# Optimization experiments

Measured on AMD Instinct MI355X. Metric: run time of the kernel, lower is better.

## Reference

```python
import jax, jax.numpy as jnp
from jax import lax
import numpy as np

B, N, D_MODEL = 4, 2048, 768
D_INNER = 1536      # int(2.0 * d_model)
DT_RANK = 48        # ceil(768 / 16)
EPS = 1e-5


def setup_inputs() -> dict:
    key = jax.random.key(0)
    ks = jax.random.split(key, 9)
    x = jax.random.normal(ks[0], (B, N, D_MODEL), jnp.float32)
    # BFS order: a permutation of node ids
    sorted_index = jax.random.permutation(ks[1], N).astype(jnp.int32)
    # parent BFS position of node at BFS position i, must be < i; root (i=0) has -1
    pos = jnp.arange(N)
    r = jax.random.randint(ks[2], (N,), 0, N)
    sorted_parent = jnp.where(pos == 0, -1, r % jnp.maximum(pos, 1)).astype(jnp.int32)
    s = 0.02
    in_proj_w = jax.random.normal(ks[3], (D_MODEL, 2 * D_INNER), jnp.float32) * s
    x_proj_w = jax.random.normal(ks[4], (D_INNER, DT_RANK + 2), jnp.float32) * s
    dt_proj_w = jax.random.normal(ks[5], (DT_RANK, D_INNER), jnp.float32) * (DT_RANK ** -0.5)
    # dt bias init: softplus^{-1}(dt) with dt ~ LogUniform(1e-3, 1e-1)
    dt = jnp.exp(jax.random.uniform(ks[6], (D_INNER,)) * (np.log(0.1) - np.log(0.001)) + np.log(0.001))
    dt_proj_b = (dt + jnp.log(-jnp.expm1(-dt))).astype(jnp.float32)
    A_log = jnp.zeros((D_INNER,), jnp.float32)   # log(A=1) per original init (d_state=1)
    D_param = jnp.ones((D_INNER,), jnp.float32)
    ln_gamma = jnp.ones((D_INNER,), jnp.float32)
    ln_beta = jnp.zeros((D_INNER,), jnp.float32)
    out_proj_w = jax.random.normal(ks[7], (D_INNER, D_MODEL), jnp.float32) * s
    return dict(x=x, sorted_index=sorted_index, sorted_parent=sorted_parent,
                in_proj_w=in_proj_w, x_proj_w=x_proj_w, dt_proj_w=dt_proj_w,
                dt_proj_b=dt_proj_b, A_log=A_log, D_param=D_param,
                ln_gamma=ln_gamma, ln_beta=ln_beta, out_proj_w=out_proj_w)


def _tree_ssm_recurrence(dBx, dA, sorted_index, sorted_parent):
    """h[bfs i] = dA[node(i)] * h[parent_bfs(i)] + dBx[node(i)]. Inputs (B,N,Di) node-major."""
    b, n, di = dBx.shape
    dA_bfs = jnp.take(dA, sorted_index, axis=1)    # (B,N,Di) in BFS order
    dBx_bfs = jnp.take(dBx, sorted_index, axis=1)

    def step(h_buf, inp):
        t, par, dA_t, dBx_t = inp                   # dA_t/dBx_t: (B,Di)
        h_par = h_buf[:, jnp.maximum(par, 0)]       # (B,Di) gather at parent BFS pos
        h_par = jnp.where(par < 0, jnp.zeros_like(h_par), h_par)
        h_t = dA_t * h_par + dBx_t
        return h_buf.at[:, t].set(h_t), h_t

    xs = (jnp.arange(n), sorted_parent,
          dA_bfs.transpose(1, 0, 2), dBx_bfs.transpose(1, 0, 2))
    _, h_bfs = lax.scan(step, jnp.zeros((b, n, di), dBx.dtype), xs)
    # scatter BFS-order states back to node-id order
    h = jnp.zeros((b, n, di), dBx.dtype).at[:, sorted_index].set(h_bfs.transpose(1, 0, 2))
    return h


def reference(x, sorted_index, sorted_parent, in_proj_w, x_proj_w, dt_proj_w,
              dt_proj_b, A_log, D_param, ln_gamma, ln_beta, out_proj_w):
    xz = x @ in_proj_w                              # (B,N,2*Di)
    x_inner, z = jnp.split(xz, 2, axis=-1)
    z = jax.nn.silu(z)
    x_dbl = x_inner @ x_proj_w                      # (B,N,dt_rank+2)
    dt_lr, B_ssm, C_ssm = (x_dbl[..., :DT_RANK], x_dbl[..., DT_RANK:DT_RANK + 1],
                           x_dbl[..., DT_RANK + 1:DT_RANK + 2])
    dt = jax.nn.softplus(dt_lr @ dt_proj_w + dt_proj_b)  # (B,N,Di)
    As = -jnp.exp(A_log)                            # (Di,) negative
    dA = jnp.exp(dt * As)                           # (B,N,Di) in (0,1)
    dBx = dt * B_ssm * x_inner                      # (B,N,Di)
    h = _tree_ssm_recurrence(dBx, dA, sorted_index, sorted_parent)
    y = h * C_ssm + D_param * x_inner               # (B,N,Di)
    mu = jnp.mean(y, axis=-1, keepdims=True)
    var = jnp.mean(jnp.square(y - mu), axis=-1, keepdims=True)
    y = (y - mu) * lax.rsqrt(var + EPS) * ln_gamma + ln_beta
    y = y * z
    return y @ out_proj_w                           # (B,N,D)
```

## Files before the change

### kernel.cpp

```cpp
#include <hip/hip_runtime.h>
#include <math.h>


#define ROWS 8192
#define DIN 1536
#define DMOD 768
#define NSEQ 2048
#define DTR 48
#define NSPLIT 4

typedef __bf16 bfrag __attribute__((ext_vector_type(8)));
typedef float f4 __attribute__((ext_vector_type(4)));

__device__ __forceinline__ unsigned short f2bf(float f) {
  unsigned int u = __float_as_uint(f);
  unsigned int r = (u + 0x7fffu + ((u >> 16) & 1u)) >> 16;
  return (unsigned short)r;
}
__device__ __forceinline__ float bf2f(unsigned short h) {
  return __uint_as_float(((unsigned int)h) << 16);
}

__device__ __forceinline__ void gld_lds16(const void* g, void* l) {
  __builtin_amdgcn_global_load_lds((const __attribute__((address_space(1))) void*)g,
                                   (__attribute__((address_space(3))) void*)l, 16, 0, 0);
}

__device__ __forceinline__ void barx() {
  asm volatile("" ::: "memory");
  __builtin_amdgcn_s_barrier();
  asm volatile("" ::: "memory");
}

__global__ __launch_bounds__(512, 1) void gemm256_silu(
    const unsigned short* __restrict__ A, const unsigned short* __restrict__ Bt,
    unsigned short* __restrict__ XI, unsigned short* __restrict__ Z, int K) {
  __shared__ unsigned short lds[2][(256 + 192) * 64];
  const int tid = threadIdx.x;
  const int w = tid >> 6, l = tid & 63;
  const int quad = l >> 4, l16 = l & 15;
  const int wr = w >> 2, wc = w & 3;
  const int h = blockIdx.x + 16 * blockIdx.y;
  const int swz = (h & 7) * 64 + (h >> 3);
  const int row0 = (swz >> 4) * 256, col0 = (swz & 15) * 192;
  const int nt = K >> 6;

  const int srow = tid >> 3;
  const int schunk = ((tid & 7) ^ (srow & 7)) * 8;
  const unsigned short* aS = A + (size_t)(row0 + srow) * K + schunk;
  const unsigned short* bS = Bt + (size_t)(col0 + srow) * K + schunk;

#define STG_A(bufi, q, kt)                                     \
  gld_lds16(aS + (size_t)((q) * 64) * K + (size_t)(kt) * 64,   \
            (char*)&lds[bufi][(q) * 4096] + w * 1024)
#define STG_B(bufi, q, kt)                                     \
  gld_lds16(bS + (size_t)((q) * 64) * K + (size_t)(kt) * 64,   \
            (char*)&lds[bufi][16384 + (q) * 4096] + w * 1024)

  const int arow = (wr * 128 + l16) * 64;
  const int brow = (wc * 48 + l16) * 64;
  int cs[2];
  cs[0] = (quad ^ (l16 & 7)) * 8;
  cs[1] = ((4 + quad) ^ (l16 & 7)) * 8;

#define RDA(m, ks) (*(const bfrag*)(const void*)(LA + arow + (m) * 1024 + cs[ks]))
#define RDB(n, ks) (*(const bfrag*)(const void*)(LB + brow + (n) * 1024 + cs[ks]))

  f4 acc[8][3];
#pragma unroll
  for (int m = 0; m < 8; m++)
#pragma unroll
    for (int n = 0; n < 3; n++) acc[m][n] = (f4){0.f, 0.f, 0.f, 0.f};

  const int kt1 = (nt > 1) ? 1 : 0;
#pragma unroll
  for (int q = 0; q < 4; q++) STG_A(0, q, 0);
#pragma unroll
  for (int q = 0; q < 3; q++) STG_B(0, q, 0);
#pragma unroll
  for (int q = 0; q < 4; q++) STG_A(1, q, kt1);
#pragma unroll
  for (int q = 0; q < 3; q++) STG_B(1, q, kt1);
  asm volatile("s_waitcnt vmcnt(7)" ::: "memory");
  barx();

  for (int t = 0; t < nt; ++t) {
    const int b = t & 1;
    const unsigned short* LA = &lds[b][0];
    const unsigned short* LB = &lds[b][16384];
    const int kA = (t + 2 < nt) ? (t + 2) : (nt - 1);
    bfrag af[4][2], bfr[3][2];

#pragma unroll
    for (int m = 0; m < 4; m++) {
      af[m][0] = RDA(m, 0);
      af[m][1] = RDA(m, 1);
    }
#pragma unroll
    for (int n = 0; n < 3; n++) {
      bfr[n][0] = RDB(n, 0);
      bfr[n][1] = RDB(n, 1);
    }
    barx();
    __builtin_amdgcn_s_setprio(1);
#pragma unroll
    for (int m = 0; m < 4; m++)
#pragma unroll
      for (int n = 0; n < 3; n++) {
        acc[m][n] = __builtin_amdgcn_mfma_f32_16x16x32_bf16(af[m][0], bfr[n][0], acc[m][n], 0, 0, 0);
        acc[m][n] = __builtin_amdgcn_mfma_f32_16x16x32_bf16(af[m][1], bfr[n][1], acc[m][n], 0, 0, 0);
      }
    __builtin_amdgcn_s_setprio(0);
    barx();

#pragma unroll
    for (int m = 0; m < 4; m++) {
      af[m][0] = RDA(m + 4, 0);
      af[m][1] = RDA(m + 4, 1);
    }
    STG_A(b, 0, kA);
    STG_A(b, 2, kA);
    STG_B(b, 0, kA);
    STG_B(b, 1, kA);
    STG_B(b, 2, kA);
    barx();
    STG_A(b, 1, kA);
    STG_A(b, 3, kA);
    __builtin_amdgcn_s_setprio(1);
#pragma unroll
    for (int m = 0; m < 4; m++)
#pragma unroll
      for (int n = 0; n < 3; n++) {
        acc[m + 4][n] = __builtin_amdgcn_mfma_f32_16x16x32_bf16(af[m][0], bfr[n][0], acc[m + 4][n], 0, 0, 0);
        acc[m + 4][n] = __builtin_amdgcn_mfma_f32_16x16x32_bf16(af[m][1], bfr[n][1], acc[m + 4][n], 0, 0, 0);
      }
    __builtin_amdgcn_s_setprio(0);
    asm volatile("s_waitcnt vmcnt(7)" ::: "memory");
    barx();
  }
  asm volatile("s_waitcnt vmcnt(0)" ::: "memory");

#undef STG_A
#undef STG_B
#undef RDA
#undef RDB

  const bool is_z = (col0 >= DIN);
  unsigned short* dst = is_z ? Z : XI;
  const int cb = col0 + wc * 48 + l16 - (is_z ? DIN : 0);
#pragma unroll
  for (int m = 0; m < 8; m++) {
    const int rb = row0 + wr * 128 + m * 16 + quad * 4;
#pragma unroll
    for (int n = 0; n < 3; n++)
#pragma unroll
      for (int r = 0; r < 4; r++) {
        float v = acc[m][n][r];
        if (is_z) v = v / (1.f + __expf(-v));
        dst[(size_t)(rb + r) * DIN + cb + n * 16] = f2bf(v);
      }
  }
}

template <int MODE>
__global__ __launch_bounds__(256) void mfma_gemm(
    const unsigned short* __restrict__ A, const unsigned short* __restrict__ Bt,
    void* __restrict__ C0v, void* __restrict__ C1v, int K, int ldc) {
  __shared__ unsigned short As[128 * 32];
  __shared__ unsigned short Bs[128 * 32];
  const int tid = threadIdx.x;
  const int w = tid >> 6, l = tid & 63;
  const int quad = l >> 4, l16 = l & 15;
  const int wrow = (w >> 1) * 64, wcol = (w & 1) * 64;
  const int h = blockIdx.x + gridDim.x * blockIdx.y;
  const int nb = gridDim.x * gridDim.y;
  int swz = h;
  if ((nb & 7) == 0) swz = (h & 7) * (nb >> 3) + (h >> 3);
  const int row0 = (swz / gridDim.x) * 128, col0 = (swz % gridDim.x) * 128;

  f4 acc[4][4];
#pragma unroll
  for (int i = 0; i < 4; i++)
#pragma unroll
    for (int j = 0; j < 4; j++) acc[i][j] = (f4){0.f, 0.f, 0.f, 0.f};

  const int arow = row0 + w * 16 + (l >> 2);
  const int brow = col0 + w * 16 + (l >> 2);
  const int kcol = (((l & 3) ^ ((l >> 2) & 3)) * 8);
  const int qs = (quad ^ (l16 & 3)) * 8;

  for (int k0 = 0; k0 < K; k0 += 32) {
#pragma unroll
    for (int r = 0; r < 2; r++) {
      gld_lds16(A + (size_t)(arow + r * 64) * K + k0 + kcol,
                (char*)As + r * 4096 + w * 1024);
      gld_lds16(Bt + (size_t)(brow + r * 64) * K + k0 + kcol,
                (char*)Bs + r * 4096 + w * 1024);
    }
    __syncthreads();
    bfrag af[4], bf[4];
#pragma unroll
    for (int i = 0; i < 4; i++)
      af[i] = *(const bfrag*)(const void*)(As + (wrow + i * 16 + l16) * 32 + qs);
#pragma unroll
    for (int j = 0; j < 4; j++)
      bf[j] = *(const bfrag*)(const void*)(Bs + (wcol + j * 16 + l16) * 32 + qs);
#pragma unroll
    for (int i = 0; i < 4; i++)
#pragma unroll
      for (int j = 0; j < 4; j++)
        acc[i][j] = __builtin_amdgcn_mfma_f32_16x16x32_bf16(af[i], bf[j], acc[i][j], 0, 0, 0);
    __syncthreads();
  }

  if (MODE == 0) {
    float* C0 = (float*)C0v;
    const int ccol = col0 + wcol + l16;
#pragma unroll
    for (int i = 0; i < 4; i++) {
      const int rb = row0 + wrow + i * 16 + quad * 4;
#pragma unroll
      for (int j = 0; j < 4; j++)
#pragma unroll
        for (int r = 0; r < 4; r++)
          C0[(size_t)(rb + r) * ldc + ccol + j * 16] = acc[i][j][r];
    }
  } else {
    const bool is_z = (col0 >= DIN);
    unsigned short* dst = is_z ? (unsigned short*)C1v : (unsigned short*)C0v;
    const int cbase = col0 + wcol + l16 - (is_z ? DIN : 0);
#pragma unroll
    for (int i = 0; i < 4; i++) {
      const int rb = row0 + wrow + i * 16 + quad * 4;
#pragma unroll
      for (int j = 0; j < 4; j++)
#pragma unroll
        for (int r = 0; r < 4; r++) {
          float v = acc[i][j][r];
          if (is_z) v = v / (1.f + __expf(-v));
          dst[(size_t)(rb + r) * DIN + cbase + j * 16] = f2bf(v);
        }
    }
  }
}

__global__ __launch_bounds__(1024) void prep1_kernel(
    const int* __restrict__ sidx, const int* __restrict__ spar,
    int* __restrict__ SLOT_PACK, int* __restrict__ SLOTINV,
    int* __restrict__ LSTART, int* __restrict__ NLEV,
    const float* __restrict__ x, unsigned short* __restrict__ Xbf,
    const float* __restrict__ xpw, unsigned short* __restrict__ XPW,
    const float* __restrict__ dtw, unsigned short* __restrict__ DTWb,
    const float* __restrict__ A_log, float* __restrict__ negA) {
  const int bi = blockIdx.x;
  const int tid = threadIdx.x;
  if (bi == 0) {
    __shared__ int par[2048], idx[2048], ancA[2048], ancB[2048], rnkA[2048], rnkB[2048];
    __shared__ int dmax;
    for (int i = tid; i < 2048; i += 1024) {
      const int p = spar[i];
      par[i] = p;
      idx[i] = sidx[i];
      ancA[i] = (p < 0) ? -1 : p;
      rnkA[i] = (p < 0) ? 0 : 1;
    }
    if (tid == 0) dmax = 0;
    __syncthreads();
    for (int r = 0; r < 11; r++) {
      int* ca = (r & 1) ? ancB : ancA;
      int* cr = (r & 1) ? rnkB : rnkA;
      int* na = (r & 1) ? ancA : ancB;
      int* nr = (r & 1) ? rnkA : rnkB;
      for (int i = tid; i < 2048; i += 1024) {
        const int a = ca[i], rv = cr[i];
        if (a >= 0) {
          nr[i] = rv + cr[a];
          na[i] = ca[a];
        } else {
          nr[i] = rv;
          na[i] = a;
        }
      }
      __syncthreads();
    }
    for (int i = tid; i < 2048; i += 1024) ancA[i] = 0;
    __syncthreads();
    for (int i = tid; i < 2048; i += 1024) {
      atomicAdd(&ancA[rnkB[i]], 1);
      atomicMax(&dmax, rnkB[i]);
    }
    __syncthreads();
    for (int s = 0; s < 11; s++) {
      const int off = 1 << s;
      int* cur = (s & 1) ? ancB : ancA;
      int* nxt = (s & 1) ? ancA : ancB;
      for (int i = tid; i < 2048; i += 1024) {
        int v = cur[i];
        if (i >= off) v += cur[i - off];
        nxt[i] = v;
      }
      __syncthreads();
    }
    for (int i = tid; i < 2049; i += 1024) {
      const int v = (i == 0) ? 0 : ancB[i - 1];
      LSTART[i] = v;
      if (i < 2048) rnkA[i] = v;
    }
    if (tid == 0) NLEV[0] = dmax + 1;
    __syncthreads();
    for (int i = tid; i < 2048; i += 1024) {
      const int d = rnkB[i];
      const int slot = atomicAdd(&rnkA[d], 1);
      const int node = idx[i];
      const int p = par[i];
      const int pn = (p < 0) ? -1 : idx[p];
      SLOT_PACK[slot] = node | ((pn + 1) << 12);
      SLOTINV[node] = slot;
    }
  } else if (bi < 1 + 1536) {
    const int i = ((bi - 1) * 1024 + tid) * 4;
    const float4 v = *(const float4*)(x + i);
    union { unsigned short h[4]; uint2 u; } pk;
    pk.h[0] = f2bf(v.x);
    pk.h[1] = f2bf(v.y);
    pk.h[2] = f2bf(v.z);
    pk.h[3] = f2bf(v.w);
    *(uint2*)(Xbf + i) = pk.u;
  } else if (bi < 1 + 1536 + 96) {
    const int i = (bi - 1537) * 1024 + tid;
    const int c = i / 1536, k = i % 1536;
    XPW[i] = (c < 50) ? f2bf(xpw[(size_t)k * 50 + c]) : (unsigned short)0;
  } else if (bi < 1 + 1536 + 96 + 96) {
    const int i = (bi - 1633) * 1024 + tid;
    const int d = i >> 6, k = i & 63;
    DTWb[i] = (k < 48) ? f2bf(dtw[(size_t)k * DIN + d]) : (unsigned short)0;
  } else {
    const int i = (bi - 1729) * 1024 + tid;
    if (i < DIN) negA[i] = -__expf(A_log[i]);
  }
}

__global__ __launch_bounds__(256) void prep2_kernel(
    const float* __restrict__ W1, unsigned short* __restrict__ W1t,
    const float* __restrict__ W2, unsigned short* __restrict__ W2t) {
  __shared__ float t[32][33];
  int idx = blockIdx.x;
  const float* W;
  unsigned short* Wt;
  int K, N, n0, k0;
  if (idx < 2304) {
    W = W1; Wt = W1t; K = DMOD; N = 2 * DIN;
    n0 = (idx % 96) * 32; k0 = (idx / 96) * 32;
  } else {
    idx -= 2304;
    W = W2; Wt = W2t; K = DIN; N = DMOD;
    n0 = (idx % 24) * 32; k0 = (idx / 24) * 32;
  }
  const int tx = threadIdx.x & 31, ty = threadIdx.x >> 5;
  for (int i = ty; i < 32; i += 8) t[i][tx] = W[(size_t)(k0 + i) * N + n0 + tx];
  __syncthreads();
  for (int i = ty; i < 32; i += 8)
    Wt[(size_t)(n0 + i) * K + k0 + tx] = f2bf(t[tx][i]);
}

__global__ __launch_bounds__(256) void xdbl_mfma(
    const unsigned short* __restrict__ XI, const unsigned short* __restrict__ XPW,
    float* __restrict__ XP) {
  __shared__ unsigned short As[128 * 32];
  __shared__ unsigned short Bs[64 * 32];
  const int tid = threadIdx.x;
  const int w = tid >> 6, l = tid & 63;
  const int quad = l >> 4, l16 = l & 15;
  const int h = blockIdx.x + 4 * blockIdx.y;
  const int swz = (h & 7) * 32 + (h >> 3);
  const int split = swz & 3;
  const int row0 = (swz >> 2) * 128;
  const int kbase = split * (DIN / NSPLIT);

  f4 acc[2][4];
#pragma unroll
  for (int i = 0; i < 2; i++)
#pragma unroll
    for (int j = 0; j < 4; j++) acc[i][j] = (f4){0.f, 0.f, 0.f, 0.f};

  const int srow = w * 16 + (l >> 2);
  const int kcol = (((l & 3) ^ ((l >> 2) & 3)) * 8);
  const int qs = (quad ^ (l16 & 3)) * 8;

  for (int c = 0; c < 12; c++) {
    const int k0 = kbase + c * 32;
#pragma unroll
    for (int r = 0; r < 2; r++) {
      gld_lds16(XI + (size_t)(row0 + srow + r * 64) * DIN + k0 + kcol,
                (char*)As + r * 4096 + w * 1024);
    }
    gld_lds16(XPW + (size_t)srow * DIN + k0 + kcol, (char*)Bs + w * 1024);
    __syncthreads();
    bfrag af[2], bf[4];
#pragma unroll
    for (int i = 0; i < 2; i++)
      af[i] = *(const bfrag*)(const void*)(As + (w * 32 + i * 16 + l16) * 32 + qs);
#pragma unroll
    for (int j = 0; j < 4; j++)
      bf[j] = *(const bfrag*)(const void*)(Bs + (j * 16 + l16) * 32 + qs);
#pragma unroll
    for (int i = 0; i < 2; i++)
#pragma unroll
      for (int j = 0; j < 4; j++)
        acc[i][j] = __builtin_amdgcn_mfma_f32_16x16x32_bf16(af[i], bf[j], acc[i][j], 0, 0, 0);
    __syncthreads();
  }

  float* dst = XP + (size_t)split * ROWS * 64 + (size_t)row0 * 64;
#pragma unroll
  for (int i = 0; i < 2; i++) {
    const int rb = w * 32 + i * 16 + quad * 4;
#pragma unroll
    for (int j = 0; j < 4; j++) {
      const int col = j * 16 + l16;
#pragma unroll
      for (int r = 0; r < 4; r++) dst[(size_t)(rb + r) * 64 + col] = acc[i][j][r];
    }
  }
}

__global__ __launch_bounds__(256) void xp_reduce(
    const float* __restrict__ XP, unsigned short* __restrict__ DTLRb,
    float* __restrict__ BCv, float* __restrict__ CCv) {
  const int i = blockIdx.x * 256 + threadIdx.x;
  const int row = i >> 4, c4 = (i & 15) * 4;
  const float* p = XP + (size_t)row * 64 + c4;
  float4 s = make_float4(0.f, 0.f, 0.f, 0.f);
#pragma unroll
  for (int sp = 0; sp < NSPLIT; sp++) {
    const float4 v = *(const float4*)(p + (size_t)sp * ROWS * 64);
    s.x += v.x;
    s.y += v.y;
    s.z += v.z;
    s.w += v.w;
  }
  if (c4 == 48) {
    BCv[row] = s.x;
    CCv[row] = s.y;
  }
  union { unsigned short h[4]; uint2 u; } pk;
  pk.h[0] = f2bf(s.x);
  pk.h[1] = f2bf(s.y);
  pk.h[2] = f2bf(s.z);
  pk.h[3] = f2bf(s.w);
  *(uint2*)(DTLRb + (size_t)row * 64 + c4) = pk.u;
}

__global__ __launch_bounds__(256) void dt_gemm(
    const unsigned short* __restrict__ DTLRb, const unsigned short* __restrict__ DTWb,
    const float* __restrict__ bias, const float* __restrict__ negA,
    const float* __restrict__ BCv, const unsigned short* __restrict__ XI,
    const int* __restrict__ SLOTINV,
    unsigned short* __restrict__ DAp, unsigned short* __restrict__ DBXp) {
  __shared__ unsigned short As[2][64 * 32];
  __shared__ unsigned short Bs[2][128 * 32];
  __shared__ int sinv[64];
  __shared__ float bcs[64];
  const int tid = threadIdx.x;
  const int w = tid >> 6, l = tid & 63;
  const int quad = l >> 4, l16 = l & 15;
  const int wrow = (w >> 1) * 32, wcol = (w & 1) * 64;
  const int h = blockIdx.x + 12 * blockIdx.y;
  const int swz = (h & 7) * 192 + (h >> 3);
  const int row0 = (swz / 12) * 64, col0 = (swz % 12) * 128;
  const int p0 = row0 & (NSEQ - 1);
  const int bbase = row0 & ~(NSEQ - 1);
  const int srow = w * 16 + (l >> 2);
  const int koff = (((l & 3) ^ ((l >> 2) & 3)) * 8);
  const int qs = (quad ^ (l16 & 3)) * 8;

#pragma unroll
  for (int c = 0; c < 2; c++) {
    gld_lds16(DTLRb + (size_t)(row0 + srow) * 64 + c * 32 + koff,
              (char*)As[c] + w * 1024);
#pragma unroll
    for (int r = 0; r < 2; r++)
      gld_lds16(DTWb + (size_t)(col0 + srow + r * 64) * 64 + c * 32 + koff,
                (char*)Bs[c] + r * 4096 + w * 1024);
  }
  if (tid < 64) {
    sinv[tid] = SLOTINV[p0 + tid];
    bcs[tid] = BCv[row0 + tid];
  }
  __syncthreads();

  f4 acc[2][4];
#pragma unroll
  for (int i = 0; i < 2; i++)
#pragma unroll
    for (int j = 0; j < 4; j++) acc[i][j] = (f4){0.f, 0.f, 0.f, 0.f};

#pragma unroll
  for (int c = 0; c < 2; c++) {
    bfrag af[2], bf[4];
#pragma unroll
    for (int i = 0; i < 2; i++)
      af[i] = *(const bfrag*)(const void*)(As[c] + (wrow + i * 16 + l16) * 32 + qs);
#pragma unroll
    for (int j = 0; j < 4; j++)
      bf[j] = *(const bfrag*)(const void*)(Bs[c] + (wcol + j * 16 + l16) * 32 + qs);
#pragma unroll
    for (int i = 0; i < 2; i++)
#pragma unroll
      for (int j = 0; j < 4; j++)
        acc[i][j] = __builtin_amdgcn_mfma_f32_16x16x32_bf16(af[i], bf[j], acc[i][j], 0, 0, 0);
  }

  float bj[4], aj[4];
#pragma unroll
  for (int j = 0; j < 4; j++) {
    const int d = col0 + wcol + j * 16 + l16;
    bj[j] = bias[d];
    aj[j] = negA[d];
  }
#pragma unroll
  for (int i = 0; i < 2; i++) {
#pragma unroll
    for (int r = 0; r < 4; r++) {
      const int row_l = wrow + i * 16 + quad * 4 + r;
      const int row = row0 + row_l;
      const float bc = bcs[row_l];
      const size_t rp = (size_t)(bbase + sinv[row_l]) * DIN;
#pragma unroll
      for (int j = 0; j < 4; j++) {
        const int d = col0 + wcol + j * 16 + l16;
        const float s = acc[i][j][r] + bj[j];
        const float sp = fmaxf(s, 0.f) + __logf(1.f + __expf(-fabsf(s)));
        const float xi = bf2f(XI[(size_t)row * DIN + d]);
        DAp[rp + d] = f2bf(__expf(sp * aj[j]));
        DBXp[rp + d] = f2bf(sp * bc * xi);
      }
    }
  }
}

__global__ __launch_bounds__(256) void recur_kernel(
    const unsigned short* __restrict__ DAp, const unsigned short* __restrict__ DBXp,
    unsigned short* __restrict__ Hb,
    const int* __restrict__ SLOT_PACK, const int* __restrict__ LSTART,
    const int* __restrict__ NLEV) {
  __shared__ unsigned short hl[NSEQ * 16];
  __shared__ int spack[NSEQ];
  __shared__ int lst[258];
  const int tid = threadIdx.x;
  const int c8a = blockIdx.x * 2;
  const int b = c8a / 192;
  const int d8a = c8a % 192;
  const int nlev = NLEV[0];
  for (int i = tid; i < NSEQ; i += 256) spack[i] = SLOT_PACK[i];
  const int nl = (nlev + 1 < 258) ? nlev + 1 : 258;
  for (int i = tid; i < nl; i += 256) lst[i] = LSTART[i];
  __syncthreads();

  for (int L = 0; L < nlev; L++) {
    const int s0 = (L < 257) ? lst[L] : LSTART[L];
    const int s1 = (L + 1 < 258) ? lst[L + 1] : LSTART[L + 1];
    const int items = (s1 - s0) * 2;
    for (int it = tid; it < items; it += 256) {
      const int s = s0 + (it >> 1);
      const int ch = it & 1;
      const size_t goff = (size_t)(b * NSEQ + s) * DIN + (d8a + ch) * 8;
      union { uint4 u; unsigned short h[8]; } da, dbx, hpu, hvu;
      da.u = *(const uint4*)(DAp + goff);
      dbx.u = *(const uint4*)(DBXp + goff);
      const int pk = spack[s];
      const int node = pk & 4095;
      const int pn = (pk >> 12) - 1;
      float hp[8];
      if (pn >= 0) {
        hpu.u = *(const uint4*)(hl + pn * 16 + ch * 8);
#pragma unroll
        for (int e = 0; e < 8; e++) hp[e] = bf2f(hpu.h[e]);
      } else {
#pragma unroll
        for (int e = 0; e < 8; e++) hp[e] = 0.f;
      }
#pragma unroll
      for (int e = 0; e < 8; e++) {
        const float hv = fmaf(bf2f(da.h[e]), hp[e], bf2f(dbx.h[e]));
        hvu.h[e] = f2bf(hv);
      }
      *(uint4*)(hl + node * 16 + ch * 8) = hvu.u;
    }
    __syncthreads();
  }

  for (int i = tid; i < NSEQ * 2; i += 256) {
    const int node = i >> 1, ch = i & 1;
    *(uint4*)(Hb + (size_t)(b * NSEQ + node) * DIN + (d8a + ch) * 8) =
        *(const uint4*)(hl + node * 16 + ch * 8);
  }
}

__global__ __launch_bounds__(256) void ln_kernel(
    const unsigned short* __restrict__ Hb, const float* __restrict__ CCv,
    const unsigned short* __restrict__ XI, const float* __restrict__ Dp,
    const float* __restrict__ gamma, const float* __restrict__ beta,
    const unsigned short* __restrict__ Z, unsigned short* __restrict__ YLN) {
  const int row = blockIdx.x;
  const int tid = threadIdx.x;
  const float C = CCv[row];
  const unsigned short* hrow = Hb + (size_t)row * DIN;
  const unsigned short* xrow = XI + (size_t)row * DIN;
  float y[6];
  float s = 0.f, s2 = 0.f;
#pragma unroll
  for (int i = 0; i < 6; i++) {
    const int d = tid + i * 256;
    const float v = fmaf(bf2f(hrow[d]), C, Dp[d] * bf2f(xrow[d]));
    y[i] = v;
    s += v;
    s2 = fmaf(v, v, s2);
  }
#pragma unroll
  for (int off = 32; off >= 1; off >>= 1) {
    s += __shfl_down(s, off);
    s2 += __shfl_down(s2, off);
  }
  __shared__ float rs[4], rs2[4];
  const int w = tid >> 6;
  if ((tid & 63) == 0) {
    rs[w] = s;
    rs2[w] = s2;
  }
  __syncthreads();
  const float ts = rs[0] + rs[1] + rs[2] + rs[3];
  const float ts2 = rs2[0] + rs2[1] + rs2[2] + rs2[3];
  const float mu = ts * (1.f / 1536.f);
  const float var = ts2 * (1.f / 1536.f) - mu * mu;
  const float inv = rsqrtf(var + 1e-5f);
  unsigned short* yrow = YLN + (size_t)row * DIN;
  const unsigned short* zrow = Z + (size_t)row * DIN;
#pragma unroll
  for (int i = 0; i < 6; i++) {
    const int d = tid + i * 256;
    const float o = (y[i] - mu) * inv * gamma[d] + beta[d];
    yrow[d] = f2bf(o * bf2f(zrow[d]));
  }
}

extern "C" void kernel_launch(void* const* d_in, const int* in_sizes, int n_in,
                              void* d_out, int out_size, void* d_ws, size_t ws_size,
                              hipStream_t stream) {
  const float* x = (const float*)d_in[0];
  const int* sidx = (const int*)d_in[1];
  const int* spar = (const int*)d_in[2];
  const float* in_proj = (const float*)d_in[3];
  const float* x_proj = (const float*)d_in[4];
  const float* dt_proj = (const float*)d_in[5];
  const float* dt_b = (const float*)d_in[6];
  const float* A_log = (const float*)d_in[7];
  const float* Dp = (const float*)d_in[8];
  const float* gamma = (const float*)d_in[9];
  const float* beta = (const float*)d_in[10];
  const float* out_proj = (const float*)d_in[11];
  float* out = (float*)d_out;

  char* p = (char*)d_ws;
  const size_t RC = (size_t)ROWS * DIN;
  unsigned short* XI = (unsigned short*)p;   p += RC * 2;
  unsigned short* Z = (unsigned short*)p;    p += RC * 2;
  unsigned short* DAp = (unsigned short*)p;  p += RC * 2;
  unsigned short* DBXp = (unsigned short*)p; p += RC * 2;
  unsigned short* Hb = (unsigned short*)p;   p += RC * 2;
  float* XP = (float*)p;                     p += (size_t)NSPLIT * ROWS * 64 * 4;
  unsigned short* DTLRb = (unsigned short*)p; p += (size_t)ROWS * 64 * 2;
  float* BCv = (float*)p;                    p += ROWS * 4;
  float* CCv = (float*)p;                    p += ROWS * 4;
  float* negA = (float*)p;                   p += DIN * 4;
  unsigned short* Xbf = (unsigned short*)p;  p += (size_t)ROWS * DMOD * 2;
  unsigned short* W1t = (unsigned short*)p;  p += (size_t)2 * DIN * DMOD * 2;
  unsigned short* W2t = (unsigned short*)p;  p += (size_t)DMOD * DIN * 2;
  unsigned short* XPW = (unsigned short*)p;  p += (size_t)64 * DIN * 2;
  unsigned short* DTWb = (unsigned short*)p; p += (size_t)DIN * 64 * 2;
  int* ipart = (int*)p;
  int* SLOT_PACK = ipart;
  int* SLOTINV = ipart + 2048;
  int* LSTART = ipart + 4096;
  int* NLEV = ipart + 4096 + 2049;
  unsigned short* YLN = DAp;

  prep1_kernel<<<1731, 1024, 0, stream>>>(sidx, spar, SLOT_PACK, SLOTINV,
                                          LSTART, NLEV, x, Xbf, x_proj, XPW,
                                          dt_proj, DTWb, A_log, negA);
  prep2_kernel<<<3456, 256, 0, stream>>>(in_proj, W1t, out_proj, W2t);
  gemm256_silu<<<dim3(16, 32), 512, 0, stream>>>(Xbf, W1t, XI, Z, DMOD);
  xdbl_mfma<<<dim3(NSPLIT, 64), 256, 0, stream>>>(XI, XPW, XP);
  xp_reduce<<<ROWS * 16 / 256, 256, 0, stream>>>(XP, DTLRb, BCv, CCv);
  dt_gemm<<<dim3(12, 128), 256, 0, stream>>>(DTLRb, DTWb, dt_b, negA, BCv, XI,
                                             SLOTINV, DAp, DBXp);
  recur_kernel<<<384, 256, 0, stream>>>(DAp, DBXp, Hb, SLOT_PACK, LSTART, NLEV);
  ln_kernel<<<ROWS, 256, 0, stream>>>(Hb, CCv, XI, Dp, gamma, beta, Z, YLN);
  mfma_gemm<0><<<dim3(6, 64), 256, 0, stream>>>(YLN, W2t, out, nullptr, DIN, DMOD);
}
```

Before: 305.3 us.

## Replace output GEMM with double-buffered 128x192 tile kernel using 512 threads

The final out-projection GEMM moves from a simple 128x128-tile, 256-thread kernel with a BK=32 synchronous load-compute loop to a new kernel. The new kernel uses 512 threads, 128x192 tiles, BK=64 and two LDS buffers, prefetching the next K tiles with global_load_lds while MFMAs run under raised wave priority. The goal is to hide global-load latency and cut per-iteration barriers for the 8192x768x1536 GEMM. The grid shrinks to 256 blocks, which on a large GPU may leave compute units underused, and the larger LDS footprint may limit occupancy.

```diff
diff --git a/kernel.cpp b/kernel.cpp
--- a/kernel.cpp
+++ b/kernel.cpp
@@ -162,85 +162,110 @@
   }
 }
 
-template <int MODE>
-__global__ __launch_bounds__(256) void mfma_gemm(
+__global__ __launch_bounds__(512, 2) void gemm_out(
     const unsigned short* __restrict__ A, const unsigned short* __restrict__ Bt,
-    void* __restrict__ C0v, void* __restrict__ C1v, int K, int ldc) {
-  __shared__ unsigned short As[128 * 32];
-  __shared__ unsigned short Bs[128 * 32];
+    float* __restrict__ C0, int K, int ldc) {
+  __shared__ unsigned short lds[2][(128 + 192) * 64];
   const int tid = threadIdx.x;
   const int w = tid >> 6, l = tid & 63;
   const int quad = l >> 4, l16 = l & 15;
-  const int wrow = (w >> 1) * 64, wcol = (w & 1) * 64;
-  const int h = blockIdx.x + gridDim.x * blockIdx.y;
-  const int nb = gridDim.x * gridDim.y;
-  int swz = h;
-  if ((nb & 7) == 0) swz = (h & 7) * (nb >> 3) + (h >> 3);
-  const int row0 = (swz / gridDim.x) * 128, col0 = (swz % gridDim.x) * 128;
-
-  f4 acc[4][4];
-#pragma unroll
-  for (int i = 0; i < 4; i++)
-#pragma unroll
-    for (int j = 0; j < 4; j++) acc[i][j] = (f4){0.f, 0.f, 0.f, 0.f};
-
-  const int arow = row0 + w * 16 + (l >> 2);
-  const int brow = col0 + w * 16 + (l >> 2);
-  const int kcol = (((l & 3) ^ ((l >> 2) & 3)) * 8);
-  const int qs = (quad ^ (l16 & 3)) * 8;
-
-  for (int k0 = 0; k0 < K; k0 += 32) {
-#pragma unroll
-    for (int r = 0; r < 2; r++) {
-      gld_lds16(A + (size_t)(arow + r * 64) * K + k0 + kcol,
-                (char*)As + r * 4096 + w * 1024);
-      gld_lds16(Bt + (size_t)(brow + r * 64) * K + k0 + kcol,
-                (char*)Bs + r * 4096 + w * 1024);
-    }
-    __syncthreads();
-    bfrag af[4], bf[4];
-#pragma unroll
-    for (int i = 0; i < 4; i++)
-      af[i] = *(const bfrag*)(const void*)(As + (wrow + i * 16 + l16) * 32 + qs);
-#pragma unroll
-    for (int j = 0; j < 4; j++)
-      bf[j] = *(const bfrag*)(const void*)(Bs + (wcol + j * 16 + l16) * 32 + qs);
-#pragma unroll
-    for (int i = 0; i < 4; i++)
-#pragma unroll
-      for (int j = 0; j < 4; j++)
-        acc[i][j] = __builtin_amdgcn_mfma_f32_16x16x32_bf16(af[i], bf[j], acc[i][j], 0, 0, 0);
-    __syncthreads();
-  }
-
-  if (MODE == 0) {
-    float* C0 = (float*)C0v;
-    const int ccol = col0 + wcol + l16;
-#pragma unroll
-    for (int i = 0; i < 4; i++) {
-      const int rb = row0 + wrow + i * 16 + quad * 4;
-#pragma unroll
-      for (int j = 0; j < 4; j++)
-#pragma unroll
-        for (int r = 0; r < 4; r++)
-          C0[(size_t)(rb + r) * ldc + ccol + j * 16] = acc[i][j][r];
-    }
-  } else {
-    const bool is_z = (col0 >= DIN);
-    unsigned short* dst = is_z ? (unsigned short*)C1v : (unsigned short*)C0v;
-    const int cbase = col0 + wcol + l16 - (is_z ? DIN : 0);
-#pragma unroll
-    for (int i = 0; i < 4; i++) {
-      const int rb = row0 + wrow + i * 16 + quad * 4;
-#pragma unroll
-      for (int j = 0; j < 4; j++)
-#pragma unroll
-        for (int r = 0; r < 4; r++) {
-          float v = acc[i][j][r];
-          if (is_z) v = v / (1.f + __expf(-v));
-          dst[(size_t)(rb + r) * DIN + cbase + j * 16] = f2bf(v);
-        }
-    }
+  const int wr = w >> 2, wc = w & 3;
+  const int h = blockIdx.x + 4 * blockIdx.y;
+  const int swz = (h & 7) * 32 + (h >> 3);
+  const int row0 = (swz >> 2) * 128, col0 = (swz & 3) * 192;
+  const int nt = K >> 6;
+
+  const int srow = tid >> 3;
+  const int schunk = ((tid & 7) ^ (srow & 7)) * 8;
+  const unsigned short* aS = A + (size_t)(row0 + srow) * K + schunk;
+  const unsigned short* bS = Bt + (size_t)(col0 + srow) * K + schunk;
+
+#define STG_A(bufi, q, kt)                                     \
+  gld_lds16(aS + (size_t)((q) * 64) * K + (size_t)(kt) * 64,   \
+            (char*)&lds[bufi][(q) * 4096] + w * 1024)
+#define STG_B(bufi, q, kt)                                     \
+  gld_lds16(bS + (size_t)((q) * 64) * K + (size_t)(kt) * 64,   \
+            (char*)&lds[bufi][8192 + (q) * 4096] + w * 1024)
+
+  const int arow = (wr * 64 + l16) * 64;
+  const int brow = (wc * 48 + l16) * 64;
+  int cs[2];
+  cs[0] = (quad ^ (l16 & 7)) * 8;
+  cs[1] = ((4 + quad) ^ (l16 & 7)) * 8;
+
+#define RDA(m, ks) (*(const bfrag*)(const void*)(LA + arow + (m) * 1024 + cs[ks]))
+#define RDB(n, ks) (*(const bfrag*)(const void*)(LB + brow + (n) * 1024 + cs[ks]))
+
+  f4 acc[4][3];
+#pragma unroll
+  for (int m = 0; m < 4; m++)
+#pragma unroll
+    for (int n = 0; n < 3; n++) acc[m][n] = (f4){0.f, 0.f, 0.f, 0.f};
+
+  const int kt1 = (nt > 1) ? 1 : 0;
+#pragma unroll
+  for (int q = 0; q < 2; q++) STG_A(0, q, 0);
+#pragma unroll
+  for (int q = 0; q < 3; q++) STG_B(0, q, 0);
+#pragma unroll
+  for (int q = 0; q < 2; q++) STG_A(1, q, kt1);
+#pragma unroll
+  for (int q = 0; q < 3; q++) STG_B(1, q, kt1);
+  asm volatile("s_waitcnt vmcnt(5)" ::: "memory");
+  barx();
+
+  for (int t = 0; t < nt; ++t) {
+    const int b = t & 1;
+    const unsigned short* LA = &lds[b][0];
+    const unsigned short* LB = &lds[b][8192];
+    const int kA = (t + 2 < nt) ? (t + 2) : (nt - 1);
+    bfrag af[4][2], bfr[3][2];
+
+#pragma unroll
+    for (int m = 0; m < 4; m++) {
+      af[m][0] = RDA(m, 0);
+      af[m][1] = RDA(m, 1);
+    }
+#pragma unroll
+    for (int n = 0; n < 3; n++) {
+      bfr[n][0] = RDB(n, 0);
+      bfr[n][1] = RDB(n, 1);
+    }
+    asm volatile("s_waitcnt lgkmcnt(0)" ::: "memory");
+    barx();
+    STG_A(b, 0, kA);
+    STG_A(b, 1, kA);
+    STG_B(b, 0, kA);
+    STG_B(b, 1, kA);
+    STG_B(b, 2, kA);
+    __builtin_amdgcn_s_setprio(1);
+#pragma unroll
+    for (int m = 0; m < 4; m++)
+#pragma unroll
+      for (int n = 0; n < 3; n++) {
+        acc[m][n] = __builtin_amdgcn_mfma_f32_16x16x32_bf16(af[m][0], bfr[n][0], acc[m][n], 0, 0, 0);
+        acc[m][n] = __builtin_amdgcn_mfma_f32_16x16x32_bf16(af[m][1], bfr[n][1], acc[m][n], 0, 0, 0);
+      }
+    __builtin_amdgcn_s_setprio(0);
+    asm volatile("s_waitcnt vmcnt(5)" ::: "memory");
+    barx();
+  }
+  asm volatile("s_waitcnt vmcnt(0)" ::: "memory");
+
+#undef STG_A
+#undef STG_B
+#undef RDA
+#undef RDB
+
+  const int cb = col0 + wc * 48 + l16;
+#pragma unroll
+  for (int m = 0; m < 4; m++) {
+    const int rb = row0 + wr * 64 + m * 16 + quad * 4;
+#pragma unroll
+    for (int n = 0; n < 3; n++)
+#pragma unroll
+      for (int r = 0; r < 4; r++)
+        C0[(size_t)(rb + r) * ldc + cb + n * 16] = acc[m][n][r];
   }
 }
 
@@ -696,5 +721,5 @@
                                              SLOTINV, DAp, DBXp);
   recur_kernel<<<384, 256, 0, stream>>>(DAp, DBXp, Hb, SLOT_PACK, LSTART, NLEV);
   ln_kernel<<<ROWS, 256, 0, stream>>>(Hb, CCv, XI, Dp, gamma, beta, Z, YLN);
-  mfma_gemm<0><<<dim3(6, 64), 256, 0, stream>>>(YLN, W2t, out, nullptr, DIN, DMOD);
-}
+  gemm_out<<<dim3(4, 64), 512, 0, stream>>>(YLN, W2t, out, DIN, DMOD);
+}
```

Result: faster. 293.6 us (-3.8%).
